# Optimization experiments

Measured on AMD Instinct MI355X. Metric: run time of the kernel, lower is better.

## Reference

```python
import jax, jax.numpy as jnp
import numpy as np
from itertools import combinations

N_COLS = 16   # number of input features (columns of xl/xu)
ADD = 3       # max subset order
ALPHA = 0.5   # primary compare weight
BETA = 0.8    # tie-break compare weight
BATCH = 65536


def _bitmask(combo):
    m = 0
    for i in combo:
        m |= 1 << i
    return m


def _build_plan(n, add):
    """Static DP plan: for each subset length, gather indices of combo[1:] (left)
    and combo[:-1] (right) among previously computed columns; plus final bitmask order."""
    items = list(range(n))
    index_dict = {(i,): i for i in items}
    count = n
    plan = []
    for length in range(2, min(add, n) + 1):
        combos = list(combinations(items, length))
        if not combos:
            continue
        left = np.array([index_dict[c[1:]] for c in combos], dtype=np.int32)
        right = np.array([index_dict[c[:-1]] for c in combos], dtype=np.int32)
        for c in combos:
            index_dict[c] = count
            count += 1
        plan.append((left, right))
    order = np.array([index_dict[c] for c in sorted(index_dict, key=_bitmask)], dtype=np.int32)
    return plan, order

_PLAN, _ORDER = _build_plan(N_COLS, ADD)


def setup_inputs() -> dict:
    key = jax.random.key(0)
    k1, k2 = jax.random.split(key)
    a = jax.random.uniform(k1, (BATCH, N_COLS), dtype=jnp.float32)
    b = jax.random.uniform(k2, (BATCH, N_COLS), dtype=jnp.float32)
    # valid intervals: xl <= xu elementwise
    xl = jnp.minimum(a, b)
    xu = jnp.maximum(a, b)
    return {"xl": xl, "xu": xu}


def _select_pair(ll, lu, rl, ru):
    # alpha-weighted score; pick the interval with SMALLER score (choose_right when cur > nxt)
    cur = (1.0 - ALPHA) * ll + ALPHA * lu
    nxt = (1.0 - ALPHA) * rl + ALPHA * ru
    # tie-break with beta-weighted score
    beta_cur = (1.0 - BETA) * ll + BETA * lu
    beta_nxt = (1.0 - BETA) * rl + BETA * ru
    choose_right = jnp.where(cur == nxt, beta_cur > beta_nxt, cur > nxt)
    res_l = jnp.where(choose_right, rl, ll)
    res_u = jnp.where(choose_right, ru, lu)
    return res_l, res_u


def reference(xl, xu):
    # mat_* grow by one block per subset length; gathers use static index arrays
    mat_l, mat_u = xl, xu
    for left_idx, right_idx in _PLAN:
        ll = mat_l[:, left_idx]
        lu = mat_u[:, left_idx]
        rl = mat_l[:, right_idx]
        ru = mat_u[:, right_idx]
        res_l, res_u = _select_pair(ll, lu, rl, ru)
        mat_l = jnp.concatenate([mat_l, res_l], axis=1)
        mat_u = jnp.concatenate([mat_u, res_u], axis=1)
    # reorder columns by subset bitmask, as in _reorder_by_bitmask
    return mat_l[:, _ORDER], mat_u[:, _ORDER]
```

## Files before the change

### kernel.cpp

```cpp
#include <hip/hip_runtime.h>
#include <cstdint>

#define NCOLS  696
#define NGROUP 174
#define RPB    4
#define BLOCK  256

struct alignas(16) Tbl { uint32_t d[NCOLS]; };

constexpr Tbl make_tbl() {
    Tbl t{};
    int p = 0;
    for (int h = 0; h < 16; ++h) {
        t.d[p++] = (uint32_t)(h | (h << 4) | (h << 8));
        for (int j = 0; j < h; ++j) {
            t.d[p++] = (uint32_t)(j | (h << 4) | (h << 8));
            for (int i = 0; i < j; ++i)
                t.d[p++] = (uint32_t)(i | (j << 4) | (h << 8));
        }
    }
    return t;
}

__constant__ Tbl g_tbl = make_tbl();

__device__ __forceinline__ float2 selpair(float2 L, float2 R) {
    float cur = __fadd_rn(__fmul_rn(0.5f, L.x), __fmul_rn(0.5f, L.y));
    float nxt = __fadd_rn(__fmul_rn(0.5f, R.x), __fmul_rn(0.5f, R.y));
    float bc  = __fadd_rn(__fmul_rn(0.2f, L.x), __fmul_rn(0.8f, L.y));
    float bn  = __fadd_rn(__fmul_rn(0.2f, R.x), __fmul_rn(0.8f, R.y));
    bool choose_right = (cur == nxt) ? (bc > bn) : (cur > nxt);
    return choose_right ? R : L;
}

__device__ __forceinline__ void col_compute(const float2* __restrict__ v,
                                            uint32_t d, float& ol, float& ou) {
    float2 Ii = v[d & 15u];
    float2 Ij = v[(d >> 4) & 15u];
    float2 Ik = v[(d >> 8) & 15u];
    float2 L = selpair(Ik, Ij);
    float2 R = selpair(Ij, Ii);
    float2 res = selpair(L, R);
    ol = res.x;
    ou = res.y;
}

__global__ __launch_bounds__(BLOCK) void minint_kernel(
    const float* __restrict__ xl, const float* __restrict__ xu,
    float* __restrict__ out, int batch)
{
    __shared__ float2 vals[RPB][16];
    const int t = threadIdx.x;
    const int base = blockIdx.x * RPB;

    if (t < RPB * 16) {
        float a = xl[base * 16 + t];
        float b = xu[base * 16 + t];
        vals[t >> 4][t & 15] = make_float2(a, b);
    }
    __syncthreads();

    const int w    = t >> 6;
    const int lane = t & 63;
    const int row  = base + w;
    const float2* v = vals[w];

    float* outl = out + (size_t)row * NCOLS;
    float* outu = out + (size_t)batch * NCOLS + (size_t)row * NCOLS;
    const uint4* tbl = (const uint4*)g_tbl.d;

    for (int g = lane; g < NGROUP; g += 64) {
        uint4 d4 = tbl[g];
        float4 rl, ru;
        col_compute(v, d4.x, rl.x, ru.x);
        col_compute(v, d4.y, rl.y, ru.y);
        col_compute(v, d4.z, rl.z, ru.z);
        col_compute(v, d4.w, rl.w, ru.w);
        *(float4*)(outl + 4 * g) = rl;
        *(float4*)(outu + 4 * g) = ru;
    }
}

extern "C" void kernel_launch(void* const* d_in, const int* in_sizes, int n_in,
                              void* d_out, int out_size, void* d_ws, size_t ws_size,
                              hipStream_t stream) {
    const float* xl = (const float*)d_in[0];
    const float* xu = (const float*)d_in[1];
    float* out = (float*)d_out;
    const int batch = in_sizes[0] / 16;
    const int grid  = batch / RPB;
    minint_kernel<<<grid, BLOCK, 0, stream>>>(xl, xu, out, batch);
}
```

Measured before the change: 392.2 us.

## Precompute pairwise selections in shared memory and use nontemporal output stores

Each block now computes the 136 singleton and pair selections per row into shared memory, so every output column needs one selpair instead of three. The column table is shrunk to 16-bit indices into that shared table. The primary score drops the 0.5 scaling, which keeps the comparison exact. Output stores become nontemporal to avoid cache pollution on the large write stream. The cost is an extra __syncthreads and more shared memory, and the kernel is likely bound by output writes anyway.

Measured after the change: 374.6 us. 4.5% less time.

```diff
diff --git a/kernel.cpp b/kernel.cpp
--- a/kernel.cpp
+++ b/kernel.cpp
@@ -3,46 +3,58 @@
 
 #define NCOLS  696
 #define NGROUP 174
+#define NREC   136
 #define RPB    4
 #define BLOCK  256
 
-struct alignas(16) Tbl { uint32_t d[NCOLS]; };
+typedef float v4f __attribute__((ext_vector_type(4)));
 
-constexpr Tbl make_tbl() {
-    Tbl t{};
+constexpr int pr(int a, int b) { return 16 + b * (b - 1) / 2 + a; }
+
+struct alignas(8) RecSrc { uint16_t d[NREC]; };
+constexpr RecSrc make_recs() {
+    RecSrc t{};
+    for (int a = 0; a < 16; ++a) t.d[a] = (uint16_t)(a | (a << 8));
+    int p = 16;
+    for (int b = 1; b < 16; ++b)
+        for (int a = 0; a < b; ++a)
+            t.d[p++] = (uint16_t)(a | (b << 8));
+    return t;
+}
+
+struct alignas(8) ColTbl { uint16_t d[NCOLS]; };
+constexpr ColTbl make_cols() {
+    ColTbl t{};
     int p = 0;
     for (int h = 0; h < 16; ++h) {
-        t.d[p++] = (uint32_t)(h | (h << 4) | (h << 8));
+        t.d[p++] = (uint16_t)(h | (h << 8));
         for (int j = 0; j < h; ++j) {
-            t.d[p++] = (uint32_t)(j | (h << 4) | (h << 8));
+            int pjh = pr(j, h);
+            t.d[p++] = (uint16_t)(pjh | (pjh << 8));
             for (int i = 0; i < j; ++i)
-                t.d[p++] = (uint32_t)(i | (j << 4) | (h << 8));
+                t.d[p++] = (uint16_t)(pr(j, h) | (pr(i, j) << 8));
         }
     }
     return t;
 }
 
-__constant__ Tbl g_tbl = make_tbl();
+__constant__ RecSrc g_recs = make_recs();
+__constant__ ColTbl g_cols = make_cols();
 
 __device__ __forceinline__ float2 selpair(float2 L, float2 R) {
-    float cur = __fadd_rn(__fmul_rn(0.5f, L.x), __fmul_rn(0.5f, L.y));
-    float nxt = __fadd_rn(__fmul_rn(0.5f, R.x), __fmul_rn(0.5f, R.y));
-    float bc  = __fadd_rn(__fmul_rn(0.2f, L.x), __fmul_rn(0.8f, L.y));
-    float bn  = __fadd_rn(__fmul_rn(0.2f, R.x), __fmul_rn(0.8f, R.y));
-    bool choose_right = (cur == nxt) ? (bc > bn) : (cur > nxt);
+    float curL = __fadd_rn(L.x, L.y);
+    float curR = __fadd_rn(R.x, R.y);
+    float bL = __fadd_rn(__fmul_rn(0.2f, L.x), __fmul_rn(0.8f, L.y));
+    float bR = __fadd_rn(__fmul_rn(0.2f, R.x), __fmul_rn(0.8f, R.y));
+    bool choose_right = (curL == curR) ? (bL > bR) : (curL > curR);
     return choose_right ? R : L;
 }
 
-__device__ __forceinline__ void col_compute(const float2* __restrict__ v,
-                                            uint32_t d, float& ol, float& ou) {
-    float2 Ii = v[d & 15u];
-    float2 Ij = v[(d >> 4) & 15u];
-    float2 Ik = v[(d >> 8) & 15u];
-    float2 L = selpair(Ik, Ij);
-    float2 R = selpair(Ij, Ii);
-    float2 res = selpair(L, R);
-    ol = res.x;
-    ou = res.y;
+__device__ __forceinline__ float2 col_compute(const float2* __restrict__ rec,
+                                              uint32_t d) {
+    float2 L = rec[d & 255u];
+    float2 R = rec[(d >> 8) & 255u];
+    return selpair(L, R);
 }
 
 __global__ __launch_bounds__(BLOCK) void minint_kernel(
@@ -50,6 +62,7 @@
     float* __restrict__ out, int batch)
 {
     __shared__ float2 vals[RPB][16];
+    __shared__ float2 recs[RPB][NREC];
     const int t = threadIdx.x;
     const int base = blockIdx.x * RPB;
 
@@ -62,22 +75,32 @@
 
     const int w    = t >> 6;
     const int lane = t & 63;
-    const int row  = base + w;
     const float2* v = vals[w];
 
+    for (int r = lane; r < NREC; r += 64) {
+        uint32_t s = g_recs.d[r];
+        float2 lo = v[s & 15u];
+        float2 hi = v[(s >> 8) & 15u];
+        recs[w][r] = selpair(hi, lo);
+    }
+    __syncthreads();
+
+    const int row = base + w;
+    const float2* rec = recs[w];
     float* outl = out + (size_t)row * NCOLS;
     float* outu = out + (size_t)batch * NCOLS + (size_t)row * NCOLS;
-    const uint4* tbl = (const uint4*)g_tbl.d;
+    const ushort4* cols = (const ushort4*)g_cols.d;
 
     for (int g = lane; g < NGROUP; g += 64) {
-        uint4 d4 = tbl[g];
-        float4 rl, ru;
-        col_compute(v, d4.x, rl.x, ru.x);
-        col_compute(v, d4.y, rl.y, ru.y);
-        col_compute(v, d4.z, rl.z, ru.z);
-        col_compute(v, d4.w, rl.w, ru.w);
-        *(float4*)(outl + 4 * g) = rl;
-        *(float4*)(outu + 4 * g) = ru;
+        ushort4 d4 = cols[g];
+        float2 c0 = col_compute(rec, d4.x);
+        float2 c1 = col_compute(rec, d4.y);
+        float2 c2 = col_compute(rec, d4.z);
+        float2 c3 = col_compute(rec, d4.w);
+        v4f rl = { c0.x, c1.x, c2.x, c3.x };
+        v4f ru = { c0.y, c1.y, c2.y, c3.y };
+        __builtin_nontemporal_store(rl, (v4f*)(outl + 4 * g));
+        __builtin_nontemporal_store(ru, (v4f*)(outu + 4 * g));
     }
 }
 
```

## Map one row per thread, stage columns in LDS, nontemporal transposed stores

Applied to the files above, without the earlier changes.

Replaces the row-per-wave column loop with a thread-per-row mapping in 64-thread blocks. Each thread computes a chunk of 32 columns into a skewed shared-memory tile, then the tile is transposed so the block writes coalesced float4 rows with nontemporal stores. The column descriptor now comes from a uniform constant load instead of a per-lane table load. The compare score is also simplified by dropping the 0.5 scaling, which leaves comparisons equivalent. Costs include a smaller block size with lower occupancy per block and more shared-memory traffic; there are no barriers around the shared tiles, which is only safe because each block is a single wavefront.

Result: slower. 527.0 us (+34.4%).

```diff
diff --git a/kernel.cpp b/kernel.cpp
--- a/kernel.cpp
+++ b/kernel.cpp
@@ -2,14 +2,17 @@
 #include <cstdint>
 
 #define NCOLS  696
-#define NGROUP 174
-#define RPB    4
-#define BLOCK  256
+#define BLOCK  64
+#define ROWS   64
+#define NCHUNK 22
+#define CHUNK  32
+#define NPAD   (NCHUNK * CHUNK)
 
-struct alignas(16) Tbl { uint32_t d[NCOLS]; };
+typedef float v4f __attribute__((ext_vector_type(4)));
 
-constexpr Tbl make_tbl() {
-    Tbl t{};
+struct alignas(16) Desc { uint32_t d[NPAD]; };
+constexpr Desc make_desc() {
+    Desc t{};
     int p = 0;
     for (int h = 0; h < 16; ++h) {
         t.d[p++] = (uint32_t)(h | (h << 4) | (h << 8));
@@ -19,65 +22,83 @@
                 t.d[p++] = (uint32_t)(i | (j << 4) | (h << 8));
         }
     }
+    for (; p < NPAD; ++p) t.d[p] = 0;
     return t;
 }
-
-__constant__ Tbl g_tbl = make_tbl();
+__constant__ Desc g_desc = make_desc();
 
 __device__ __forceinline__ float2 selpair(float2 L, float2 R) {
-    float cur = __fadd_rn(__fmul_rn(0.5f, L.x), __fmul_rn(0.5f, L.y));
-    float nxt = __fadd_rn(__fmul_rn(0.5f, R.x), __fmul_rn(0.5f, R.y));
-    float bc  = __fadd_rn(__fmul_rn(0.2f, L.x), __fmul_rn(0.8f, L.y));
-    float bn  = __fadd_rn(__fmul_rn(0.2f, R.x), __fmul_rn(0.8f, R.y));
-    bool choose_right = (cur == nxt) ? (bc > bn) : (cur > nxt);
+    float curL = __fadd_rn(L.x, L.y);
+    float curR = __fadd_rn(R.x, R.y);
+    float bL = __fadd_rn(__fmul_rn(0.2f, L.x), __fmul_rn(0.8f, L.y));
+    float bR = __fadd_rn(__fmul_rn(0.2f, R.x), __fmul_rn(0.8f, R.y));
+    bool choose_right = (curL == curR) ? (bL > bR) : (curL > curR);
     return choose_right ? R : L;
-}
-
-__device__ __forceinline__ void col_compute(const float2* __restrict__ v,
-                                            uint32_t d, float& ol, float& ou) {
-    float2 Ii = v[d & 15u];
-    float2 Ij = v[(d >> 4) & 15u];
-    float2 Ik = v[(d >> 8) & 15u];
-    float2 L = selpair(Ik, Ij);
-    float2 R = selpair(Ij, Ii);
-    float2 res = selpair(L, R);
-    ol = res.x;
-    ou = res.y;
 }
 
 __global__ __launch_bounds__(BLOCK) void minint_kernel(
     const float* __restrict__ xl, const float* __restrict__ xu,
     float* __restrict__ out, int batch)
 {
-    __shared__ float2 vals[RPB][16];
-    const int t = threadIdx.x;
-    const int base = blockIdx.x * RPB;
+    __shared__ float2 iv[16 * 64];
+    __shared__ float2 st[CHUNK * 64];
+    const int r = threadIdx.x;
+    const size_t row = (size_t)blockIdx.x * ROWS + r;
 
-    if (t < RPB * 16) {
-        float a = xl[base * 16 + t];
-        float b = xu[base * 16 + t];
-        vals[t >> 4][t & 15] = make_float2(a, b);
-    }
-    __syncthreads();
+    const float4* pl = (const float4*)(xl + row * 16);
+    const float4* pu = (const float4*)(xu + row * 16);
+    float4 a0 = pl[0], a1 = pl[1], a2 = pl[2], a3 = pl[3];
+    float4 b0 = pu[0], b1 = pu[1], b2 = pu[2], b3 = pu[3];
+    iv[ 0*64 + r] = make_float2(a0.x, b0.x);
+    iv[ 1*64 + r] = make_float2(a0.y, b0.y);
+    iv[ 2*64 + r] = make_float2(a0.z, b0.z);
+    iv[ 3*64 + r] = make_float2(a0.w, b0.w);
+    iv[ 4*64 + r] = make_float2(a1.x, b1.x);
+    iv[ 5*64 + r] = make_float2(a1.y, b1.y);
+    iv[ 6*64 + r] = make_float2(a1.z, b1.z);
+    iv[ 7*64 + r] = make_float2(a1.w, b1.w);
+    iv[ 8*64 + r] = make_float2(a2.x, b2.x);
+    iv[ 9*64 + r] = make_float2(a2.y, b2.y);
+    iv[10*64 + r] = make_float2(a2.z, b2.z);
+    iv[11*64 + r] = make_float2(a2.w, b2.w);
+    iv[12*64 + r] = make_float2(a3.x, b3.x);
+    iv[13*64 + r] = make_float2(a3.y, b3.y);
+    iv[14*64 + r] = make_float2(a3.z, b3.z);
+    iv[15*64 + r] = make_float2(a3.w, b3.w);
 
-    const int w    = t >> 6;
-    const int lane = t & 63;
-    const int row  = base + w;
-    const float2* v = vals[w];
+    const size_t row0 = (size_t)blockIdx.x * ROWS;
+    float* outl = out + row0 * NCOLS;
+    float* outu = out + (size_t)batch * NCOLS + row0 * NCOLS;
 
-    float* outl = out + (size_t)row * NCOLS;
-    float* outu = out + (size_t)batch * NCOLS + (size_t)row * NCOLS;
-    const uint4* tbl = (const uint4*)g_tbl.d;
-
-    for (int g = lane; g < NGROUP; g += 64) {
-        uint4 d4 = tbl[g];
-        float4 rl, ru;
-        col_compute(v, d4.x, rl.x, ru.x);
-        col_compute(v, d4.y, rl.y, ru.y);
-        col_compute(v, d4.z, rl.z, ru.z);
-        col_compute(v, d4.w, rl.w, ru.w);
-        *(float4*)(outl + 4 * g) = rl;
-        *(float4*)(outu + 4 * g) = ru;
+    int C = 0;
+    for (int ch = 0; ch < NCHUNK; ++ch, C += CHUNK) {
+        #pragma unroll 4
+        for (int c = 0; c < CHUNK; ++c) {
+            uint32_t d = g_desc.d[C + c];
+            float2 Ii = iv[(d & 15u) * 64 + r];
+            float2 Ij = iv[((d >> 4) & 15u) * 64 + r];
+            float2 Ih = iv[((d >> 8) & 15u) * 64 + r];
+            float2 res = selpair(selpair(Ih, Ij), selpair(Ij, Ii));
+            st[c * 64 + ((r + c) & 63)] = res;
+        }
+        const int ncq = (ch == NCHUNK - 1) ? 6 : 8;
+        const int cq = r & 7;
+        #pragma unroll
+        for (int q = 0; q < 8; ++q) {
+            const int rr = (r >> 3) + q * 8;
+            if (cq < ncq) {
+                const int c0 = cq * 4;
+                float2 e0 = st[(c0 + 0) * 64 + ((rr + c0 + 0) & 63)];
+                float2 e1 = st[(c0 + 1) * 64 + ((rr + c0 + 1) & 63)];
+                float2 e2 = st[(c0 + 2) * 64 + ((rr + c0 + 2) & 63)];
+                float2 e3 = st[(c0 + 3) * 64 + ((rr + c0 + 3) & 63)];
+                v4f vl = { e0.x, e1.x, e2.x, e3.x };
+                v4f vu = { e0.y, e1.y, e2.y, e3.y };
+                const size_t off = (size_t)rr * NCOLS + (C + c0);
+                __builtin_nontemporal_store(vl, (v4f*)(outl + off));
+                __builtin_nontemporal_store(vu, (v4f*)(outu + off));
+            }
+        }
     }
 }
 
@@ -88,6 +109,6 @@
     const float* xu = (const float*)d_in[1];
     float* out = (float*)d_out;
     const int batch = in_sizes[0] / 16;
-    const int grid  = batch / RPB;
+    const int grid  = batch / ROWS;
     minint_kernel<<<grid, BLOCK, 0, stream>>>(xl, xu, out, batch);
 }
```
